# Kernel tuning notes

Measured on AMD Instinct MI355X. Metric: run time of the kernel, lower is better.

The kernel has to match this reference:

```python
import jax, jax.numpy as jnp
import numpy as np

V, L, H, D, T, B = 32000, 8, 16, 1024, 1024, 2
HD = D // H
SCALE = 1.0 / float(np.sqrt(HD))


def setup_inputs() -> dict:
    key = jax.random.key(0)
    ks = jax.random.split(key, 8)
    s = 0.02
    def n(k, shape):
        return jax.random.normal(k, shape, jnp.float32) * s
    return {
        "input_ids": jax.random.randint(ks[0], (B, T), 0, V),
        "tok_emb": n(ks[1], (V, D)),            # tied with lm_head
        "pos_emb": n(ks[2], (T, D)),
        "ln1_w": jnp.ones((L, D)), "ln1_b": jnp.zeros((L, D)),
        "qkv_w": n(ks[3], (L, D, 3 * D)),       # no bias in qkv_proj
        "out_w": n(ks[4], (L, D, D)), "out_b": jnp.zeros((L, D)),
        "ln2_w": jnp.ones((L, D)), "ln2_b": jnp.zeros((L, D)),
        "fc1_w": n(ks[5], (L, D, 4 * D)), "fc1_b": jnp.zeros((L, 4 * D)),
        "fc2_w": n(ks[6], (L, 4 * D, D)), "fc2_b": jnp.zeros((L, D)),
        "lnf_w": jnp.ones((D,)), "lnf_b": jnp.zeros((D,)),
    }


def _ln(x, w, b):
    m = x.mean(-1, keepdims=True)
    v = x.var(-1, keepdims=True)
    return (x - m) * jax.lax.rsqrt(v + 1e-5) * w + b


def _gpt(input_ids, tok_emb, pos_emb, ln1_w, ln1_b, qkv_w, out_w, out_b,
         ln2_w, ln2_b, fc1_w, fc1_b, fc2_w, fc2_b, lnf_w, lnf_b):
    Bq, Tq = input_ids.shape
    x = tok_emb[input_ids] + pos_emb[:Tq][None]          # [B,T,D]
    causal = jnp.tril(jnp.ones((Tq, Tq), bool))          # [T,T]

    def layer(x, p):
        l1w, l1b, qw, ow, ob, l2w, l2b, f1w, f1b, f2w, f2b = p
        h = _ln(x, l1w, l1b)
        qkv = h @ qw                                     # [B,T,3D]
        q, k, v = jnp.split(qkv, 3, axis=-1)
        q = q.reshape(Bq, Tq, H, HD)
        k = k.reshape(Bq, Tq, H, HD)
        v = v.reshape(Bq, Tq, H, HD)
        att = jnp.einsum('bqhd,bkhd->bhqk', q, k) * SCALE
        att = jnp.where(causal, att, -jnp.inf)
        att = jax.nn.softmax(att, axis=-1)
        o = jnp.einsum('bhqk,bkhd->bqhd', att, v).reshape(Bq, Tq, D)
        x = x + o @ ow + ob
        h2 = _ln(x, l2w, l2b)
        x = x + jax.nn.gelu(h2 @ f1w + f1b, approximate=False) @ f2w + f2b
        return x, None

    x, _ = jax.lax.scan(layer, x, (ln1_w, ln1_b, qkv_w, out_w, out_b,
                                   ln2_w, ln2_b, fc1_w, fc1_b, fc2_w, fc2_b))
    x = _ln(x, lnf_w, lnf_b)
    return x @ tok_emb.T                                 # tied lm_head


def reference(input_ids, tok_emb, pos_emb, ln1_w, ln1_b, qkv_w, out_w, out_b,
              ln2_w, ln2_b, fc1_w, fc1_b, fc2_w, fc2_b, lnf_w, lnf_b):
    return _gpt(input_ids, tok_emb, pos_emb, ln1_w, ln1_b, qkv_w, out_w, out_b,
                ln2_w, ln2_b, fc1_w, fc1_b, fc2_w, fc2_b, lnf_w, lnf_b)
```

## Files before the change

kernel.cpp:

```cpp
#include <hip/hip_runtime.h>
#include <hip/hip_bf16.h>
#include <math.h>


#define DEV_INLINE __device__ __forceinline__

typedef float  f32x4  __attribute__((ext_vector_type(4)));
typedef __bf16 bf16x8 __attribute__((ext_vector_type(8)));
typedef short  s16x4  __attribute__((ext_vector_type(4)));
typedef short  s16x8  __attribute__((ext_vector_type(8)));
typedef unsigned int u32x4 __attribute__((ext_vector_type(4)));

#define BBATCH 2
#define TSEQ   1024
#define DMODEL 1024
#define NHEAD  16
#define HDIM   64
#define NLAYER 8
#define NVOCAB 32000
#define MTOK   (BBATCH*TSEQ)

DEV_INLINE short f2bf(float f) {
    __bf16 h = (__bf16)f;
    union { __bf16 h; short s; } u; u.h = h; return u.s;
}

typedef const __attribute__((address_space(1))) unsigned int* gas_t;
typedef __attribute__((address_space(3))) unsigned int* las_t;
DEV_INLINE void llds16(const void* g, void* l) {
    __builtin_amdgcn_global_load_lds((gas_t)g, (las_t)l, 16, 0, 0);
}

#define BAR()  asm volatile("s_barrier" ::: "memory")
#define VMW4() asm volatile("s_waitcnt vmcnt(4)" ::: "memory")
#define VMW2() asm volatile("s_waitcnt vmcnt(2)" ::: "memory")
#define VMW0() asm volatile("s_waitcnt vmcnt(0)" ::: "memory")

DEV_INLINE float block_sum(float v) {
    __shared__ float sb[4];
    #pragma unroll
    for (int o = 32; o > 0; o >>= 1) v += __shfl_down(v, o, 64);
    if ((threadIdx.x & 63) == 0) sb[threadIdx.x >> 6] = v;
    __syncthreads();
    float r = sb[0] + sb[1] + sb[2] + sb[3];
    __syncthreads();
    return r;
}

__global__ __launch_bounds__(256) void flash_k(
    const short* __restrict__ qkv, const short* __restrict__ Vt,
    short* __restrict__ O)
{
    const int qb = blockIdx.x;
    const int z  = blockIdx.y;
    const int zb = z >> 4, zh = z & 15;

    __shared__ short Qs[128 * 64];
    __shared__ short KP[128 * 136];
    __shared__ short Vs[64 * 128];

    const int tid  = threadIdx.x;
    const int w    = tid >> 6, lane = tid & 63;
    const int lr   = lane & 15, kg = lane >> 4;

    const long long qbase = (long long)zb * TSEQ * 3072;
    const short* Qg = qkv + qbase + zh * HDIM;
    const short* Kg = qkv + qbase + DMODEL + zh * HDIM;
    const short* Vg = Vt + (long long)z * (HDIM * TSEQ);

    const int sr   = tid >> 3, pc = tid & 7;
    const int lc   = pc ^ (sr & 7);
    const int sr16 = tid >> 4, pc16 = tid & 15;

    {
        const short* qp = Qg + (long long)(qb * 128 + sr) * 3072 + lc * 8;
        const short* kp = Kg + (long long)(0 + sr) * 3072 + lc * 8;
        #pragma unroll
        for (int it = 0; it < 4; ++it) {
            llds16(qp + (long long)it * 32 * 3072, Qs + tid * 8 + it * 2048);
            llds16(kp + (long long)it * 32 * 3072, KP + tid * 8 + it * 2048);
        }
        #pragma unroll
        for (int it = 0; it < 4; ++it) {
            const int r = it * 16 + sr16;
            const int lc2 = pc16 ^ (r & 7);
            llds16(Vg + (long long)r * TSEQ + 0 + lc2 * 8, Vs + tid * 8 + it * 2048);
        }
    }
    __syncthreads();
    bf16x8 afq[2][2];
    #pragma unroll
    for (int s = 0; s < 2; ++s)
        #pragma unroll
        for (int i = 0; i < 2; ++i) {
            const int r = w * 32 + i * 16 + lr;
            afq[s][i] = *(const bf16x8*)&Qs[r * 64 + (((s * 4 + kg) ^ (r & 7)) << 3)];
        }

    f32x4 aco[2][4] = {};
    float m_[2][4], l_[2][4];
    #pragma unroll
    for (int i = 0; i < 2; ++i)
        #pragma unroll
        for (int p = 0; p < 4; ++p) { m_[i][p] = -1e30f; l_[i][p] = 0.f; }

    const int nt = qb + 1;
    for (int t = 0; t < nt; ++t) {
        u32x4 kpre[4], vpre[4];
        const bool nx = (t + 1 < nt);
        if (nx) {
            const int kn = (t + 1) * 128;
            #pragma unroll
            for (int it = 0; it < 4; ++it)
                kpre[it] = *(const u32x4*)(Kg + (long long)(kn + sr + it * 32) * 3072 + lc * 8);
            #pragma unroll
            for (int it = 0; it < 4; ++it) {
                const int r = it * 16 + sr16;
                const int lc2 = pc16 ^ (r & 7);
                vpre[it] = *(const u32x4*)(Vg + (long long)r * TSEQ + kn + lc2 * 8);
            }
            __builtin_amdgcn_sched_barrier(0);
        }

        f32x4 acs[2][8] = {};
        #pragma unroll
        for (int s = 0; s < 2; ++s)
            #pragma unroll
            for (int j = 0; j < 8; ++j) {
                const int rk = j * 16 + lr;
                bf16x8 bk = *(const bf16x8*)&KP[rk * 64 + (((s * 4 + kg) ^ (rk & 7)) << 3)];
                #pragma unroll
                for (int i = 0; i < 2; ++i)
                    acs[i][j] = __builtin_amdgcn_mfma_f32_16x16x32_bf16(
                        afq[s][i], bk, acs[i][j], 0, 0, 0);
            }

        #pragma unroll
        for (int i = 0; i < 2; ++i)
            #pragma unroll
            for (int j = 0; j < 8; ++j)
                #pragma unroll
                for (int p = 0; p < 4; ++p) {
                    float v = acs[i][j][p] * 0.125f;
                    if (t == qb && (j * 16 + lr) > (w * 32 + i * 16 + kg * 4 + p))
                        v = -1e30f;
                    acs[i][j][p] = v;
                }

        float sc[2][4];
        #pragma unroll
        for (int i = 0; i < 2; ++i)
            #pragma unroll
            for (int p = 0; p < 4; ++p) {
                float r = acs[i][0][p];
                #pragma unroll
                for (int j = 1; j < 8; ++j) r = fmaxf(r, acs[i][j][p]);
                r = fmaxf(r, __shfl_xor(r, 1, 64));
                r = fmaxf(r, __shfl_xor(r, 2, 64));
                r = fmaxf(r, __shfl_xor(r, 4, 64));
                r = fmaxf(r, __shfl_xor(r, 8, 64));
                const float mn = fmaxf(m_[i][p], r);
                sc[i][p] = __expf(m_[i][p] - mn);
                m_[i][p] = mn;
            }
        #pragma unroll
        for (int i = 0; i < 2; ++i)
            #pragma unroll
            for (int j = 0; j < 8; ++j)
                #pragma unroll
                for (int p = 0; p < 4; ++p)
                    acs[i][j][p] = __expf(acs[i][j][p] - m_[i][p]);
        #pragma unroll
        for (int i = 0; i < 2; ++i)
            #pragma unroll
            for (int p = 0; p < 4; ++p) {
                float s = 0.f;
                #pragma unroll
                for (int j = 0; j < 8; ++j) s += acs[i][j][p];
                s += __shfl_xor(s, 1, 64);
                s += __shfl_xor(s, 2, 64);
                s += __shfl_xor(s, 4, 64);
                s += __shfl_xor(s, 8, 64);
                l_[i][p] = l_[i][p] * sc[i][p] + s;
            }
        #pragma unroll
        for (int i = 0; i < 2; ++i)
            #pragma unroll
            for (int j2 = 0; j2 < 4; ++j2)
                #pragma unroll
                for (int p = 0; p < 4; ++p)
                    aco[i][j2][p] *= sc[i][p];

        __syncthreads();

        #pragma unroll
        for (int i = 0; i < 2; ++i)
            #pragma unroll
            for (int j = 0; j < 8; ++j)
                #pragma unroll
                for (int p = 0; p < 4; ++p)
                    KP[(w * 32 + i * 16 + kg * 4 + p) * 136 + j * 16 + lr] =
                        f2bf(acs[i][j][p]);
        __syncthreads();

        #pragma unroll
        for (int ks = 0; ks < 4; ++ks) {
            bf16x8 pa[2], pb[4];
            #pragma unroll
            for (int i = 0; i < 2; ++i)
                pa[i] = *(const bf16x8*)&KP[(w * 32 + i * 16 + lr) * 136 + ks * 32 + kg * 8];
            #pragma unroll
            for (int j2 = 0; j2 < 4; ++j2) {
                const int d = j2 * 16 + lr;
                pb[j2] = *(const bf16x8*)&Vs[d * 128 + (((ks * 4 + kg) ^ (d & 7)) << 3)];
            }
            #pragma unroll
            for (int i = 0; i < 2; ++i)
                #pragma unroll
                for (int j2 = 0; j2 < 4; ++j2)
                    aco[i][j2] = __builtin_amdgcn_mfma_f32_16x16x32_bf16(
                        pa[i], pb[j2], aco[i][j2], 0, 0, 0);
        }
        __syncthreads();

        if (nx) {
            #pragma unroll
            for (int it = 0; it < 4; ++it)
                *(u32x4*)(KP + tid * 8 + it * 2048) = kpre[it];
            #pragma unroll
            for (int it = 0; it < 4; ++it)
                *(u32x4*)(Vs + tid * 8 + it * 2048) = vpre[it];
            __syncthreads();
        }
    }

    #pragma unroll
    for (int i = 0; i < 2; ++i)
        #pragma unroll
        for (int j2 = 0; j2 < 4; ++j2)
            #pragma unroll
            for (int p = 0; p < 4; ++p) {
                const int row = zb * TSEQ + qb * 128 + w * 32 + i * 16 + kg * 4 + p;
                const int col = zh * HDIM + j2 * 16 + lr;
                O[(long long)row * DMODEL + col] = f2bf(aco[i][j2][p] / l_[i][p]);
            }
}

__global__ __launch_bounds__(512, 2) void gemm256_k(
    const short* __restrict__ A, const short* __restrict__ B,
    float* __restrict__ C, int K, int lda, int ldb, int ldc, int gx)
{
    extern __shared__ short smem[];

    const int nwg = gridDim.x;
    int wg = blockIdx.x;
    int sw = (wg & 7) * (nwg >> 3) + (wg >> 3);
    const int bx = sw >> 3, by = sw & 7;
    const int bn0 = bx * 256, bm0 = by * 256;

    const int tid  = threadIdx.x;
    const int w    = tid >> 6, lane = tid & 63;
    const int wm   = w >> 2, wn = w & 3;
    const int lr   = lane & 15, kg = lane >> 4;

    const int r0  = tid >> 3;
    const int pc  = tid & 7;
    const int lc0 = pc ^ (r0 & 7);
    const int r1  = r0 + 64;
    const int lc1 = pc ^ (r1 & 7);

    f32x4 acc[2][2][4][2] = {};
    const int nk = K >> 6;

    auto stage = [&](int buf, int isA, int h, int kk) {
        const short* gp = isA ? A : B;
        const int    ld = isA ? lda : ldb;
        const long long rb = (long long)((isA ? bm0 : bn0) + h * 128);
        short* lp = smem + buf * 32768 + (isA ? 0 : 16384) + h * 8192;
        llds16(gp + (rb + r0) * ld + kk + lc0 * 8, lp + w * 512);
        llds16(gp + (rb + r1) * ld + kk + lc1 * 8, lp + 4096 + w * 512);
    };

#define PHASE(BUF, QM, QN, ISA, H, DOWAIT)                                      \
    do {                                                                        \
        const short* Ah = smem + (BUF) * 32768 + (QM) * 8192;                   \
        const short* Bh = smem + (BUF) * 32768 + 16384 + (QN) * 8192;           \
        bf16x8 af[2][4], bfr[2][2];                                             \
        _Pragma("unroll")                                                       \
        for (int s2 = 0; s2 < 2; ++s2) {                                        \
            _Pragma("unroll")                                                   \
            for (int i = 0; i < 4; ++i) {                                       \
                const int ra = wm * 64 + i * 16 + lr;                           \
                af[s2][i] = *(const bf16x8*)                                    \
                    &Ah[ra * 64 + (((s2 * 4 + kg) ^ (ra & 7)) << 3)];           \
            }                                                                   \
            _Pragma("unroll")                                                   \
            for (int j = 0; j < 2; ++j) {                                       \
                const int rb2 = wn * 32 + j * 16 + lr;                          \
                bfr[s2][j] = *(const bf16x8*)                                   \
                    &Bh[rb2 * 64 + (((s2 * 4 + kg) ^ (rb2 & 7)) << 3)];         \
            }                                                                   \
        }                                                                       \
        if (pf) stage(nb, ISA, H, kk);                                          \
        BAR();                                                                  \
        __builtin_amdgcn_s_setprio(1);                                          \
        _Pragma("unroll")                                                       \
        for (int s2 = 0; s2 < 2; ++s2)                                          \
            _Pragma("unroll")                                                   \
            for (int i = 0; i < 4; ++i)                                         \
                _Pragma("unroll")                                               \
                for (int j = 0; j < 2; ++j)                                     \
                    acc[QM][QN][i][j] = __builtin_amdgcn_mfma_f32_16x16x32_bf16(\
                        af[s2][i], bfr[s2][j], acc[QM][QN][i][j], 0, 0, 0);     \
        __builtin_amdgcn_s_setprio(0);                                          \
        DOWAIT;                                                                 \
        BAR();                                                                  \
    } while (0)

    stage(0, 1, 0, 0);
    stage(0, 0, 0, 0);
    stage(0, 1, 1, 0);
    stage(0, 0, 1, 0);
    if (nk > 1) { VMW4(); } else { VMW0(); }
    BAR();

    for (int t = 0; t < nk - 1; ++t) {
        const int  buf = t & 1, nb = buf ^ 1;
        const int  kk  = (t + 1) << 6;
        const bool pf  = true;
        PHASE(buf, 0, 0, 1, 0, VMW4());
        PHASE(buf, 1, 0, 0, 0, VMW4());
        PHASE(buf, 1, 1, 1, 1, (void)0);
        PHASE(buf, 0, 1, 0, 1, VMW4());
    }
    {
        const int  buf = (nk - 1) & 1, nb = buf ^ 1; (void)nb;
        const int  kk  = 0;
        const bool pf  = false;
        PHASE(buf, 0, 0, 1, 0, VMW2());
        PHASE(buf, 1, 0, 0, 0, VMW0());
        PHASE(buf, 1, 1, 1, 1, (void)0);
        PHASE(buf, 0, 1, 0, 1, (void)0);
    }
#undef PHASE

    #pragma unroll
    for (int qm = 0; qm < 2; ++qm)
        #pragma unroll
        for (int qn = 0; qn < 2; ++qn)
            #pragma unroll
            for (int i = 0; i < 4; ++i)
                #pragma unroll
                for (int j = 0; j < 2; ++j) {
                    const int gr = bm0 + qm * 128 + wm * 64 + i * 16 + kg * 4;
                    const int gc = bn0 + qn * 128 + wn * 32 + j * 16 + lr;
                    #pragma unroll
                    for (int p = 0; p < 4; ++p)
                        C[(long long)(gr + p) * ldc + gc] = acc[qm][qn][i][j][p];
                }
}

template<int BN, int EPI>
__global__ __launch_bounds__(256) void gemm_k(
    const short* __restrict__ Ag, const short* __restrict__ Bg,
    void* __restrict__ Cg, const float* __restrict__ bias,
    int M, int N, int K, int lda, int ldb, int ldc,
    long long sAz, long long sBz, long long sCz,
    float scale, int swz)
{
    int bx = blockIdx.x, by = blockIdx.y;
    if (swz) {
        const int gx = gridDim.x;
        const int nwg = gx * gridDim.y;
        if ((nwg & 7) == 0) {
            int wg = by * gx + bx;
            int wg2 = (wg & 7) * (nwg >> 3) + (wg >> 3);
            bx = wg2 % gx; by = wg2 / gx;
        }
    }
    const int bn0 = bx * BN, bm0 = by * 128;
    const int zz = blockIdx.z;

    const short* A = Ag + zz * sAz;
    const short* B = Bg + zz * sBz;

    __shared__ short Als[2][128 * 64];
    __shared__ short Bls[2][BN * 64];

    const int tid  = threadIdx.x;
    const int lane = tid & 63;
    const int wave = tid >> 6;
    constexpr int WMS = (BN == 128) ? 64 : 32;
    constexpr int MI  = (BN == 128) ? 4 : 2;
    constexpr int NJ  = 4;
    const int wm = (BN == 128) ? (wave >> 1) : wave;
    const int wn = (BN == 128) ? (wave & 1) : 0;
    const int lr = lane & 15, kg = lane >> 4;
    const int xv = (lr & 7) << 4;

    const int sr = tid >> 3;
    const int sc = (tid & 7) ^ (sr & 7);
    const short* aP = A + (long long)(bm0 + sr) * lda + sc * 8;
    const short* bP = B + (long long)(bn0 + sr) * ldb + sc * 8;

    f32x4 acc[MI][NJ] = {};
    const int nk = K >> 6;

    auto stage = [&](int buf, int kt) {
        const int k0 = kt << 6;
        short* aL = &Als[buf][wave * 512];
        short* bL = &Bls[buf][wave * 512];
        #pragma unroll
        for (int it = 0; it < 4; ++it)
            llds16(aP + (long long)it * 32 * lda + k0, aL + it * 2048);
        #pragma unroll
        for (int it = 0; it < BN / 32; ++it)
            llds16(bP + (long long)it * 32 * ldb + k0, bL + it * 2048);
    };

    stage(0, 0);
    __syncthreads();

    for (int kt = 0; kt < nk; ++kt) {
        const int cb = kt & 1;
        if (kt + 1 < nk) stage(cb ^ 1, kt + 1);

        #pragma unroll
        for (int s = 0; s < 2; ++s) {
            const int ofs = (((s << 6) | (kg << 4)) ^ xv) >> 1;
            bf16x8 af[MI], bf[NJ];
            #pragma unroll
            for (int i = 0; i < MI; ++i)
                af[i] = *(const bf16x8*)&Als[cb][(wm * WMS + i * 16 + lr) * 64 + ofs];
            #pragma unroll
            for (int j = 0; j < NJ; ++j)
                bf[j] = *(const bf16x8*)&Bls[cb][(wn * 64 + j * 16 + lr) * 64 + ofs];
            #pragma unroll
            for (int i = 0; i < MI; ++i)
                #pragma unroll
                for (int j = 0; j < NJ; ++j)
                    acc[i][j] = __builtin_amdgcn_mfma_f32_16x16x32_bf16(
                        af[i], bf[j], acc[i][j], 0, 0, 0);
        }
        __syncthreads();
    }

    short* Cs = (short*)Cg + zz * sCz;
    float* Cf = (float*)Cg + zz * sCz;
    #pragma unroll
    for (int i = 0; i < MI; ++i) {
        #pragma unroll
        for (int j = 0; j < NJ; ++j) {
            const int gr = bm0 + wm * WMS + i * 16 + kg * 4;
            const int gc = bn0 + wn * 64 + j * 16 + lr;
            #pragma unroll
            for (int p = 0; p < 4; ++p) {
                const long long off = (long long)(gr + p) * ldc + gc;
                float v = acc[i][j][p];
                if (EPI == 0) {
                    Cf[off] = v;
                } else if (EPI == 1) {
                    Cs[off] = f2bf(v * scale);
                } else {
                    v += bias[gc];
                    v = 0.5f * v * (1.0f + erff(v * 0.70710678118654752f));
                    Cs[off] = f2bf(v);
                }
            }
        }
    }
}

__global__ __launch_bounds__(256) void fredln_k(
    const float* __restrict__ p0, const float* __restrict__ p1,
    const float* __restrict__ bias, float* __restrict__ x,
    const float* __restrict__ lw, const float* __restrict__ lb,
    short* __restrict__ o)
{
    const int row = blockIdx.x;
    const long long base = (long long)row * DMODEL;
    const int i = threadIdx.x * 4;
    float4 a  = *(const float4*)&p0[base + i];
    float4 b  = *(const float4*)&p1[base + i];
    float4 c  = *(const float4*)&x[base + i];
    float4 bb = *(const float4*)&bias[i];
    float4 v;
    v.x = c.x + a.x + b.x + bb.x;
    v.y = c.y + a.y + b.y + bb.y;
    v.z = c.z + a.z + b.z + bb.z;
    v.w = c.w + a.w + b.w + bb.w;
    *(float4*)&x[base + i] = v;
    float s  = v.x + v.y + v.z + v.w;
    float s2 = v.x * v.x + v.y * v.y + v.z * v.z + v.w * v.w;
    s  = block_sum(s);
    s2 = block_sum(s2);
    const float mean = s * (1.0f / DMODEL);
    const float var  = s2 * (1.0f / DMODEL) - mean * mean;
    const float rs   = rsqrtf(var + 1e-5f);
    float4 wv = *(const float4*)&lw[i];
    float4 bv = *(const float4*)&lb[i];
    s16x4 ov;
    ov[0] = f2bf((v.x - mean) * rs * wv.x + bv.x);
    ov[1] = f2bf((v.y - mean) * rs * wv.y + bv.y);
    ov[2] = f2bf((v.z - mean) * rs * wv.z + bv.z);
    ov[3] = f2bf((v.w - mean) * rs * wv.w + bv.w);
    *(s16x4*)&o[base + i] = ov;
}

__global__ __launch_bounds__(256) void embedln_k(
    const int* __restrict__ ids, const float* __restrict__ tok,
    const float* __restrict__ pos, float* __restrict__ x,
    const float* __restrict__ lw, const float* __restrict__ lb,
    short* __restrict__ o)
{
    const int row = blockIdx.x;
    const int t   = row & (TSEQ - 1);
    const int id  = ids[row];
    const int i   = threadIdx.x * 4;
    const long long base = (long long)row * DMODEL;
    float4 a = *(const float4*)&tok[(long long)id * DMODEL + i];
    float4 p = *(const float4*)&pos[(long long)t * DMODEL + i];
    float4 v;
    v.x = a.x + p.x; v.y = a.y + p.y; v.z = a.z + p.z; v.w = a.w + p.w;
    *(float4*)&x[base + i] = v;
    float s  = v.x + v.y + v.z + v.w;
    float s2 = v.x * v.x + v.y * v.y + v.z * v.z + v.w * v.w;
    s  = block_sum(s);
    s2 = block_sum(s2);
    const float mean = s * (1.0f / DMODEL);
    const float var  = s2 * (1.0f / DMODEL) - mean * mean;
    const float rs   = rsqrtf(var + 1e-5f);
    float4 wv = *(const float4*)&lw[i];
    float4 bv = *(const float4*)&lb[i];
    s16x4 ov;
    ov[0] = f2bf((v.x - mean) * rs * wv.x + bv.x);
    ov[1] = f2bf((v.y - mean) * rs * wv.y + bv.y);
    ov[2] = f2bf((v.z - mean) * rs * wv.z + bv.z);
    ov[3] = f2bf((v.w - mean) * rs * wv.w + bv.w);
    *(s16x4*)&o[base + i] = ov;
}

template<typename T>
DEV_INLINE void tcvt_body(const T* sp, short* dp, int lds_, int ldd,
                          int bx, int by, short (*ls)[68], int t)
{
    const int tr0 = by * 64, tc0 = bx * 64;
    const int rr = t >> 4, cc = (t & 15) * 4;
    #pragma unroll
    for (int q = 0; q < 4; ++q) {
        const int r = q * 16 + rr;
        if constexpr (sizeof(T) == 4) {
            float4 v = *(const float4*)&sp[(long long)(tr0 + r) * lds_ + tc0 + cc];
            ls[cc + 0][r] = f2bf(v.x); ls[cc + 1][r] = f2bf(v.y);
            ls[cc + 2][r] = f2bf(v.z); ls[cc + 3][r] = f2bf(v.w);
        } else {
            s16x4 v = *(const s16x4*)&sp[(long long)(tr0 + r) * lds_ + tc0 + cc];
            ls[cc + 0][r] = v[0]; ls[cc + 1][r] = v[1];
            ls[cc + 2][r] = v[2]; ls[cc + 3][r] = v[3];
        }
    }
    __syncthreads();
    #pragma unroll
    for (int q = 0; q < 4; ++q) {
        const int c = q * 16 + rr;
        s16x4 v;
        v[0] = ls[c][cc]; v[1] = ls[c][cc + 1]; v[2] = ls[c][cc + 2]; v[3] = ls[c][cc + 3];
        *(s16x4*)&dp[(long long)(tc0 + c) * ldd + tr0 + cc] = v;
    }
}

template<typename T>
__global__ __launch_bounds__(256) void tcvt_k(
    const T* __restrict__ src, short* __restrict__ dst,
    int lds_, int ldd, int Hdiv,
    long long sSb, long long sSh, long long sDb, long long sDh)
{
    __shared__ short ls[64][68];
    const int z = blockIdx.z, zb = z / Hdiv, zh = z - zb * Hdiv;
    tcvt_body<T>(src + zb * sSb + zh * sSh, dst + zb * sDb + zh * sDh,
                 lds_, ldd, blockIdx.x, blockIdx.y, ls, threadIdx.x);
}

__global__ __launch_bounds__(256) void wcvt_k(
    const float* __restrict__ qw, const float* __restrict__ ow,
    const float* __restrict__ f1, const float* __restrict__ f2,
    short* __restrict__ wq, short* __restrict__ wo,
    short* __restrict__ w1, short* __restrict__ w2)
{
    __shared__ short ls[64][68];
    const int id = blockIdx.x;
    const float* src; short* dst; int lds_, ldd, bx, by;
    if (id < 768)       { src = qw; dst = wq; lds_ = 3072; ldd = 1024; bx = id % 48;  by = id / 48; }
    else if (id < 1024) { int i = id - 768;  src = ow; dst = wo; lds_ = 1024; ldd = 1024; bx = i % 16; by = i / 16; }
    else if (id < 2048) { int i = id - 1024; src = f1; dst = w1; lds_ = 4096; ldd = 1024; bx = i % 64; by = i / 64; }
    else                { int i = id - 2048; src = f2; dst = w2; lds_ = 1024; ldd = 4096; bx = i % 16; by = i / 16; }
    tcvt_body<float>(src, dst, lds_, ldd, bx, by, ls, threadIdx.x);
}

__global__ __launch_bounds__(256) void cvt_k(
    const float* __restrict__ s, short* __restrict__ d, int n4)
{
    int i = blockIdx.x * 256 + threadIdx.x;
    const int stride = gridDim.x * 256;
    for (; i < n4; i += stride) {
        float4 v = *(const float4*)&s[(long long)i * 4];
        s16x4 o = { f2bf(v.x), f2bf(v.y), f2bf(v.z), f2bf(v.w) };
        *(s16x4*)&d[(long long)i * 4] = o;
    }
}

extern "C" void kernel_launch(void* const* d_in, const int* in_sizes, int n_in,
                              void* d_out, int out_size, void* d_ws, size_t ws_size,
                              hipStream_t stream)
{
    const int*   ids  = (const int*)  d_in[0];
    const float* tok  = (const float*)d_in[1];
    const float* pos  = (const float*)d_in[2];
    const float* ln1w = (const float*)d_in[3];
    const float* ln1b = (const float*)d_in[4];
    const float* qkvw = (const float*)d_in[5];
    const float* outw = (const float*)d_in[6];
    const float* outb = (const float*)d_in[7];
    const float* ln2w = (const float*)d_in[8];
    const float* ln2b = (const float*)d_in[9];
    const float* fc1w = (const float*)d_in[10];
    const float* fc1b = (const float*)d_in[11];
    const float* fc2w = (const float*)d_in[12];
    const float* fc2b = (const float*)d_in[13];
    const float* lnfw = (const float*)d_in[14];
    const float* lnfb = (const float*)d_in[15];
    float* out = (float*)d_out;

    char* ws = (char*)d_ws;
    const size_t MB = 1024 * 1024;
    float* x    = (float*)(ws);
    short* hb   = (short*)(ws + 8  * MB);
    short* qkvb = (short*)(ws + 12 * MB);
    short* g    = (short*)(ws + 24 * MB);
    short* Vt   = (short*)(ws + 40 * MB);
    float* fp   = (float*)(ws + 44 * MB);
    short* tokb = (short*)(ws + 12 * MB);

    const bool big = ws_size >= (size_t)267 * MB;
    short* wq = (short*)(ws + 75 * MB);
    short *wo, *w1, *w2;
    if (big) {
        wo = (short*)(ws + 123 * MB);
        w1 = (short*)(ws + 139 * MB);
        w2 = (short*)(ws + 203 * MB);
    } else {
        wo = (short*)(ws + 81 * MB);
        w1 = (short*)(ws + 83 * MB);
        w2 = (short*)(ws + 91 * MB);
    }

    const long long LWQ = 3072LL * 1024, LWO = 1024LL * 1024;
    const long long LW1 = 4096LL * 1024, LW2 = 1024LL * 4096;
    const long long MD  = (long long)MTOK * DMODEL;

    hipFuncSetAttribute((const void*)gemm256_k,
                        hipFuncAttributeMaxDynamicSharedMemorySize, 131072);

    dim3 blk(256);
    embedln_k<<<MTOK, blk, 0, stream>>>(ids, tok, pos, x, ln1w, ln1b, hb);

    if (big) {
        tcvt_k<float><<<dim3(48, 16, 8), blk, 0, stream>>>(qkvw, wq, 3072, 1024, 1, LWQ, 0, LWQ, 0);
        tcvt_k<float><<<dim3(16, 16, 8), blk, 0, stream>>>(outw, wo, 1024, 1024, 1, LWO, 0, LWO, 0);
        tcvt_k<float><<<dim3(64, 16, 8), blk, 0, stream>>>(fc1w, w1, 4096, 1024, 1, LW1, 0, LW1, 0);
        tcvt_k<float><<<dim3(16, 64, 8), blk, 0, stream>>>(fc2w, w2, 1024, 4096, 1, LW2, 0, LW2, 0);
    }

    for (int l = 0; l < NLAYER; ++l) {
        short* wql = wq + (big ? l * LWQ : 0);
        short* wol = wo + (big ? l * LWO : 0);
        short* w1l = w1 + (big ? l * LW1 : 0);
        short* w2l = w2 + (big ? l * LW2 : 0);
        if (!big)
            wcvt_k<<<3072, blk, 0, stream>>>(
                qkvw + l * LWQ, outw + l * LWO, fc1w + l * LW1, fc2w + l * LW2,
                wql, wol, w1l, w2l);

        gemm_k<128, 1><<<dim3(24, 16, 1), blk, 0, stream>>>(
            hb, wql, qkvb, nullptr,
            MTOK, 3 * DMODEL, DMODEL, DMODEL, DMODEL, 3 * DMODEL,
            0, 0, 0, 1.0f, 1);

        tcvt_k<short><<<dim3(1, 16, BBATCH * NHEAD), blk, 0, stream>>>(
            qkvb + 2 * DMODEL, Vt, 3 * DMODEL, TSEQ, NHEAD,
            (long long)TSEQ * 3 * DMODEL, HDIM,
            (long long)NHEAD * HDIM * TSEQ, (long long)HDIM * TSEQ);

        flash_k<<<dim3(8, BBATCH * NHEAD), blk, 0, stream>>>(qkvb, Vt, hb);

        gemm_k<128, 0><<<dim3(8, 16, 2), blk, 0, stream>>>(
            hb, wol, fp, nullptr,
            MTOK, DMODEL, 512, DMODEL, DMODEL, DMODEL,
            512, 512, MD, 1.0f, 1);
        fredln_k<<<MTOK, blk, 0, stream>>>(
            fp, fp + MD, outb + l * DMODEL, x,
            ln2w + l * DMODEL, ln2b + l * DMODEL, hb);

        gemm_k<128, 3><<<dim3(32, 16, 1), blk, 0, stream>>>(
            hb, w1l, g, fc1b + (long long)l * 4 * DMODEL,
            MTOK, 4 * DMODEL, DMODEL, DMODEL, DMODEL, 4 * DMODEL,
            0, 0, 0, 1.0f, 1);

        gemm_k<128, 0><<<dim3(8, 16, 2), blk, 0, stream>>>(
            g, w2l, fp, nullptr,
            MTOK, DMODEL, 2048, 4 * DMODEL, 4 * DMODEL, DMODEL,
            2048, 2048, MD, 1.0f, 1);
        const float* nlw = (l < 7) ? ln1w + (l + 1) * DMODEL : lnfw;
        const float* nlb = (l < 7) ? ln1b + (l + 1) * DMODEL : lnfb;
        fredln_k<<<MTOK, blk, 0, stream>>>(
            fp, fp + MD, fc2b + l * DMODEL, x, nlw, nlb, hb);
    }

    cvt_k<<<2048, blk, 0, stream>>>(tok, tokb, NVOCAB * DMODEL / 4);

    gemm256_k<<<dim3((NVOCAB / 256) * (MTOK / 256)), dim3(512), 131072, stream>>>(
        hb, tokb, out, DMODEL, DMODEL, DMODEL, NVOCAB, NVOCAB / 256);
}
```

Measured before the change: 1.675 ms.

## Fuse V transpose into QKV GEMM epilogue, widen FC2 split-K, warp-per-row LN

```diff
diff --git a/kernel.cpp b/kernel.cpp
--- a/kernel.cpp
+++ b/kernel.cpp
@@ -364,6 +364,7 @@
 __global__ __launch_bounds__(256) void gemm_k(
     const short* __restrict__ Ag, const short* __restrict__ Bg,
     void* __restrict__ Cg, const float* __restrict__ bias,
+    short* __restrict__ aux,
     int M, int N, int K, int lda, int ldb, int ldc,
     long long sAz, long long sBz, long long sCz,
     float scale, int swz)
@@ -453,58 +454,84 @@
         for (int j = 0; j < NJ; ++j) {
             const int gr = bm0 + wm * WMS + i * 16 + kg * 4;
             const int gc = bn0 + wn * 64 + j * 16 + lr;
-            #pragma unroll
-            for (int p = 0; p < 4; ++p) {
-                const long long off = (long long)(gr + p) * ldc + gc;
-                float v = acc[i][j][p];
-                if (EPI == 0) {
-                    Cf[off] = v;
-                } else if (EPI == 1) {
-                    Cs[off] = f2bf(v * scale);
-                } else {
-                    v += bias[gc];
-                    v = 0.5f * v * (1.0f + erff(v * 0.70710678118654752f));
-                    Cs[off] = f2bf(v);
+            if (EPI == 4 && gc >= 2 * DMODEL) {
+                const int b = gr >> 10, t0 = gr & (TSEQ - 1);
+                const int h = (gc - 2 * DMODEL) >> 6, d = gc & 63;
+                s16x4 vv;
+                #pragma unroll
+                for (int p = 0; p < 4; ++p) vv[p] = f2bf(acc[i][j][p]);
+                *(s16x4*)&aux[((long long)(b * NHEAD + h) * HDIM + d) * TSEQ + t0] = vv;
+            } else {
+                #pragma unroll
+                for (int p = 0; p < 4; ++p) {
+                    const long long off = (long long)(gr + p) * ldc + gc;
+                    float v = acc[i][j][p];
+                    if (EPI == 0) {
+                        Cf[off] = v;
+                    } else if (EPI == 1 || EPI == 4) {
+                        Cs[off] = f2bf(v * scale);
+                    } else {
+                        v += bias[gc];
+                        v = 0.5f * v * (1.0f + erff(v * 0.70710678118654752f));
+                        Cs[off] = f2bf(v);
+                    }
                 }
             }
         }
     }
 }
 
+template<int NP>
 __global__ __launch_bounds__(256) void fredln_k(
-    const float* __restrict__ p0, const float* __restrict__ p1,
+    const float* __restrict__ fp, long long pstride,
     const float* __restrict__ bias, float* __restrict__ x,
     const float* __restrict__ lw, const float* __restrict__ lb,
     short* __restrict__ o)
 {
-    const int row = blockIdx.x;
-    const long long base = (long long)row * DMODEL;
-    const int i = threadIdx.x * 4;
-    float4 a  = *(const float4*)&p0[base + i];
-    float4 b  = *(const float4*)&p1[base + i];
-    float4 c  = *(const float4*)&x[base + i];
-    float4 bb = *(const float4*)&bias[i];
-    float4 v;
-    v.x = c.x + a.x + b.x + bb.x;
-    v.y = c.y + a.y + b.y + bb.y;
-    v.z = c.z + a.z + b.z + bb.z;
-    v.w = c.w + a.w + b.w + bb.w;
-    *(float4*)&x[base + i] = v;
-    float s  = v.x + v.y + v.z + v.w;
-    float s2 = v.x * v.x + v.y * v.y + v.z * v.z + v.w * v.w;
-    s  = block_sum(s);
-    s2 = block_sum(s2);
+    const int row  = blockIdx.x * 4 + (threadIdx.x >> 6);
+    const int lane = threadIdx.x & 63;
+    const long long base = (long long)row * DMODEL + lane * 16;
+    const int cb = lane * 16;
+    float4 v[4];
+    #pragma unroll
+    for (int q = 0; q < 4; ++q) {
+        v[q] = *(const float4*)&x[base + q * 4];
+        float4 bb = *(const float4*)&bias[cb + q * 4];
+        v[q].x += bb.x; v[q].y += bb.y; v[q].z += bb.z; v[q].w += bb.w;
+        #pragma unroll
+        for (int k = 0; k < NP; ++k) {
+            float4 pp = *(const float4*)&fp[k * pstride + base + q * 4];
+            v[q].x += pp.x; v[q].y += pp.y; v[q].z += pp.z; v[q].w += pp.w;
+        }
+        *(float4*)&x[base + q * 4] = v[q];
+    }
+    float s = 0.f, s2 = 0.f;
+    #pragma unroll
+    for (int q = 0; q < 4; ++q) {
+        s  += v[q].x + v[q].y + v[q].z + v[q].w;
+        s2 += v[q].x * v[q].x + v[q].y * v[q].y + v[q].z * v[q].z + v[q].w * v[q].w;
+    }
+    #pragma unroll
+    for (int d = 1; d < 64; d <<= 1) {
+        s  += __shfl_xor(s, d, 64);
+        s2 += __shfl_xor(s2, d, 64);
+    }
     const float mean = s * (1.0f / DMODEL);
     const float var  = s2 * (1.0f / DMODEL) - mean * mean;
     const float rs   = rsqrtf(var + 1e-5f);
-    float4 wv = *(const float4*)&lw[i];
-    float4 bv = *(const float4*)&lb[i];
-    s16x4 ov;
-    ov[0] = f2bf((v.x - mean) * rs * wv.x + bv.x);
-    ov[1] = f2bf((v.y - mean) * rs * wv.y + bv.y);
-    ov[2] = f2bf((v.z - mean) * rs * wv.z + bv.z);
-    ov[3] = f2bf((v.w - mean) * rs * wv.w + bv.w);
-    *(s16x4*)&o[base + i] = ov;
+    short ov[16];
+    #pragma unroll
+    for (int q = 0; q < 4; ++q) {
+        float4 wv = *(const float4*)&lw[cb + q * 4];
+        float4 bv = *(const float4*)&lb[cb + q * 4];
+        ov[q * 4 + 0] = f2bf((v[q].x - mean) * rs * wv.x + bv.x);
+        ov[q * 4 + 1] = f2bf((v[q].y - mean) * rs * wv.y + bv.y);
+        ov[q * 4 + 2] = f2bf((v[q].z - mean) * rs * wv.z + bv.z);
+        ov[q * 4 + 3] = f2bf((v[q].w - mean) * rs * wv.w + bv.w);
+    }
+    short* op = o + base;
+    *(s16x8*)op       = *(s16x8*)&ov[0];
+    *(s16x8*)(op + 8) = *(s16x8*)&ov[8];
 }
 
 __global__ __launch_bounds__(256) void embedln_k(
@@ -641,17 +668,17 @@
     float* fp   = (float*)(ws + 44 * MB);
     short* tokb = (short*)(ws + 12 * MB);
 
-    const bool big = ws_size >= (size_t)267 * MB;
-    short* wq = (short*)(ws + 75 * MB);
+    const bool big = ws_size >= (size_t)272 * MB;
+    short* wq = (short*)(ws + 80 * MB);
     short *wo, *w1, *w2;
     if (big) {
-        wo = (short*)(ws + 123 * MB);
-        w1 = (short*)(ws + 139 * MB);
-        w2 = (short*)(ws + 203 * MB);
+        wo = (short*)(ws + 128 * MB);
+        w1 = (short*)(ws + 144 * MB);
+        w2 = (short*)(ws + 208 * MB);
     } else {
-        wo = (short*)(ws + 81 * MB);
-        w1 = (short*)(ws + 83 * MB);
-        w2 = (short*)(ws + 91 * MB);
+        wo = (short*)(ws + 86 * MB);
+        w1 = (short*)(ws + 88 * MB);
+        w2 = (short*)(ws + 96 * MB);
     }
 
     const long long LWQ = 3072LL * 1024, LWO = 1024LL * 1024;
@@ -681,39 +708,34 @@
                 qkvw + l * LWQ, outw + l * LWO, fc1w + l * LW1, fc2w + l * LW2,
                 wql, wol, w1l, w2l);
 
-        gemm_k<128, 1><<<dim3(24, 16, 1), blk, 0, stream>>>(
-            hb, wql, qkvb, nullptr,
+        gemm_k<128, 4><<<dim3(24, 16, 1), blk, 0, stream>>>(
+            hb, wql, qkvb, nullptr, Vt,
             MTOK, 3 * DMODEL, DMODEL, DMODEL, DMODEL, 3 * DMODEL,
             0, 0, 0, 1.0f, 1);
 
-        tcvt_k<short><<<dim3(1, 16, BBATCH * NHEAD), blk, 0, stream>>>(
-            qkvb + 2 * DMODEL, Vt, 3 * DMODEL, TSEQ, NHEAD,
-            (long long)TSEQ * 3 * DMODEL, HDIM,
-            (long long)NHEAD * HDIM * TSEQ, (long long)HDIM * TSEQ);
-
         flash_k<<<dim3(8, BBATCH * NHEAD), blk, 0, stream>>>(qkvb, Vt, hb);
 
         gemm_k<128, 0><<<dim3(8, 16, 2), blk, 0, stream>>>(
-            hb, wol, fp, nullptr,
+            hb, wol, fp, nullptr, nullptr,
             MTOK, DMODEL, 512, DMODEL, DMODEL, DMODEL,
             512, 512, MD, 1.0f, 1);
-        fredln_k<<<MTOK, blk, 0, stream>>>(
-            fp, fp + MD, outb + l * DMODEL, x,
+        fredln_k<2><<<MTOK / 4, blk, 0, stream>>>(
+            fp, MD, outb + l * DMODEL, x,
             ln2w + l * DMODEL, ln2b + l * DMODEL, hb);
 
         gemm_k<128, 3><<<dim3(32, 16, 1), blk, 0, stream>>>(
-            hb, w1l, g, fc1b + (long long)l * 4 * DMODEL,
+            hb, w1l, g, fc1b + (long long)l * 4 * DMODEL, nullptr,
             MTOK, 4 * DMODEL, DMODEL, DMODEL, DMODEL, 4 * DMODEL,
             0, 0, 0, 1.0f, 1);
 
-        gemm_k<128, 0><<<dim3(8, 16, 2), blk, 0, stream>>>(
-            g, w2l, fp, nullptr,
-            MTOK, DMODEL, 2048, 4 * DMODEL, 4 * DMODEL, DMODEL,
-            2048, 2048, MD, 1.0f, 1);
+        gemm_k<128, 0><<<dim3(8, 16, 4), blk, 0, stream>>>(
+            g, w2l, fp, nullptr, nullptr,
+            MTOK, DMODEL, 1024, 4 * DMODEL, 4 * DMODEL, DMODEL,
+            1024, 1024, MD, 1.0f, 1);
         const float* nlw = (l < 7) ? ln1w + (l + 1) * DMODEL : lnfw;
         const float* nlb = (l < 7) ? ln1b + (l + 1) * DMODEL : lnfb;
-        fredln_k<<<MTOK, blk, 0, stream>>>(
-            fp, fp + MD, fc2b + l * DMODEL, x, nlw, nlb, hb);
+        fredln_k<4><<<MTOK / 4, blk, 0, stream>>>(
+            fp, MD, fc2b + l * DMODEL, x, nlw, nlb, hb);
     }
 
     cvt_k<<<2048, blk, 0, stream>>>(tok, tokb, NVOCAB * DMODEL / 4);
```

New measurement: 1.585 ms. 1.06x faster.
